# Performance work log

Measured on AMD Instinct MI355X. Metric: run time of the kernel, lower is better.

## Reference

```python
import jax, jax.numpy as jnp
import numpy as np

B, S, D, H = 2, 2048, 1024, 16
DH = D // H
ROPE_BASE = 10000.0


def apply_rope(x):
    # x: [B, H, S, DH]; rotate-half RoPE, base 10000
    half = DH // 2
    inv_freq = 1.0 / (ROPE_BASE ** (jnp.arange(half, dtype=jnp.float32) / half))
    ang = jnp.arange(S, dtype=jnp.float32)[:, None] * inv_freq[None, :]  # [S, half]
    cos = jnp.cos(ang)[None, None]  # [1,1,S,half]
    sin = jnp.sin(ang)[None, None]
    x1, x2 = x[..., :half], x[..., half:]
    return jnp.concatenate([x1 * cos - x2 * sin, x1 * sin + x2 * cos], axis=-1)


def setup_inputs() -> dict:
    key = jax.random.key(0)
    ks = jax.random.split(key, 9)
    w = lambda k: jax.random.normal(k, (D, D), dtype=jnp.float32) * 0.02
    return {
        "x": jax.random.normal(ks[0], (B, S, D), dtype=jnp.float32),
        "Wq": w(ks[1]), "bq": jnp.zeros((D,), jnp.float32),
        "Wk": w(ks[2]), "bk": jnp.zeros((D,), jnp.float32),
        "Wv": w(ks[3]), "bv": jnp.zeros((D,), jnp.float32),
        "Wo": w(ks[4]), "bo": jnp.zeros((D,), jnp.float32),
    }


def reference(x, Wq, bq, Wk, bk, Wv, bv, Wo, bo):
    # projections (W stored as [in, out])
    q = x @ Wq + bq
    k = x @ Wk + bk
    v = x @ Wv + bv
    # [B, S, D] -> [B, H, S, DH]
    to_heads = lambda t: t.reshape(B, S, H, DH).transpose(0, 2, 1, 3)
    q, k, v = to_heads(q), to_heads(k), to_heads(v)
    q = apply_rope(q)
    k = apply_rope(k)
    scores = jnp.einsum("bhqd,bhkd->bhqk", q, k) / jnp.sqrt(jnp.float32(DH))
    causal = jnp.tril(jnp.ones((S, S), dtype=bool))  # [S, S]
    scores = jnp.where(causal[None, None], scores, -jnp.inf)
    probs = jax.nn.softmax(scores, axis=-1)
    ctx = jnp.einsum("bhqk,bhkd->bhqd", probs, v)
    ctx = ctx.transpose(0, 2, 1, 3).reshape(B, S, D)  # concat heads
    return ctx @ Wo + bo
```

## Files before the change

kernel.cpp:

```cpp
#include <hip/hip_runtime.h>
#include <hip/hip_bf16.h>

#define B_  2
#define S_  2048
#define D_  1024
#define H_  16
#define DH_ 64

typedef __attribute__((ext_vector_type(8))) short bf16x8;
typedef __attribute__((ext_vector_type(4))) float f32x4;

__device__ __forceinline__ short f2bf(float f) {
  unsigned int u; __builtin_memcpy(&u, &f, 4);
  u = (u + 0x7FFFu + ((u >> 16) & 1u)) >> 16;
  return (short)u;
}
__device__ __forceinline__ unsigned cvtpk(float a, float b) {
  unsigned r;
  asm("v_cvt_pk_bf16_f32 %0, %1, %2" : "=v"(r) : "v"(a), "v"(b));
  return r;
}

#define GLOAD_LDS16(gp, lp) \
  __builtin_amdgcn_global_load_lds((const __attribute__((address_space(1))) void*)(gp), \
                                   (__attribute__((address_space(3))) void*)(lp), 16, 0, 0)

#define MFMA16(a, b, c) __builtin_amdgcn_mfma_f32_16x16x32_bf16(a, b, c, 0, 0, 0)

union U8 { unsigned u[4]; bf16x8 v; };

__global__ __launch_bounds__(256) void k_cvt(const float* __restrict__ in,
                                             short* __restrict__ out, int n4) {
  int i = blockIdx.x * 256 + threadIdx.x;
  if (i >= n4) return;
  float4 v = ((const float4*)in)[i];
  short4 o; o.x = f2bf(v.x); o.y = f2bf(v.y); o.z = f2bf(v.z); o.w = f2bf(v.w);
  *(short4*)(out + (size_t)i * 4) = o;
}

__global__ __launch_bounds__(256) void k_transpose(const float* __restrict__ W,
                                                   short* __restrict__ Wt) {
  __shared__ float tile[32][33];
  int tx = threadIdx.x, ty = threadIdx.y;
  int bx = blockIdx.x * 32, by = blockIdx.y * 32;
  #pragma unroll
  for (int i = 0; i < 32; i += 8)
    tile[ty + i][tx] = W[(size_t)(by + ty + i) * D_ + bx + tx];
  __syncthreads();
  #pragma unroll
  for (int i = 0; i < 32; i += 8)
    Wt[(size_t)(bx + ty + i) * D_ + by + tx] = f2bf(tile[tx][ty + i]);
}

__global__ __launch_bounds__(256) void k_rope_table(float* __restrict__ cosT,
                                                    float* __restrict__ sinT) {
  int i = blockIdx.x * 256 + threadIdx.x;
  int s = i >> 5, d = i & 31;
  float invf = exp2f(-(float)d * (13.287712379549449f / 32.0f));
  float ang = (float)s * invf;
  cosT[i] = cosf(ang);
  sinT[i] = sinf(ang);
}

__global__ __launch_bounds__(256) void k_gemm_qkv(const short* __restrict__ A,
                                                  const short* __restrict__ Bt,
                                                  const float* __restrict__ bq,
                                                  const float* __restrict__ bk,
                                                  const float* __restrict__ bv,
                                                  const float* __restrict__ cosT,
                                                  const float* __restrict__ sinT,
                                                  short* __restrict__ qb,
                                                  short* __restrict__ kb,
                                                  short* __restrict__ vb) {
  const int K = 1024;
  __shared__ __align__(16) short lA[128 * 32];
  __shared__ __align__(16) short lB[128 * 32];
  const int tid = threadIdx.x;
  const int wid = tid >> 6, lane = tid & 63;
  const int brow = blockIdx.y * 128, bcol = blockIdx.x * 128;
  const int wr = wid >> 1, wc = wid & 1;
  const int g = lane >> 4, c15 = lane & 15;
  const int sr = lane >> 2, scol = (lane & 3) * 8;
  f32x4 acc[4][4] = {};

  for (int kt = 0; kt < K; kt += 32) {
    __syncthreads();
    #pragma unroll
    for (int ch = 0; ch < 2; ++ch) {
      const short* ga = A + (size_t)(brow + ch * 64 + wid * 16 + sr) * K + kt + scol;
      const short* gb = Bt + (size_t)(bcol + ch * 64 + wid * 16 + sr) * K + kt + scol;
      GLOAD_LDS16(ga, &lA[(ch * 64 + wid * 16) * 32]);
      GLOAD_LDS16(gb, &lB[(ch * 64 + wid * 16) * 32]);
    }
    __syncthreads();
    bf16x8 af[4], bfr[4];
    #pragma unroll
    for (int mi = 0; mi < 4; ++mi)
      af[mi] = *(const bf16x8*)&lA[(wr * 64 + mi * 16 + c15) * 32 + g * 8];
    #pragma unroll
    for (int ni = 0; ni < 4; ++ni)
      bfr[ni] = *(const bf16x8*)&lB[(wc * 64 + ni * 16 + c15) * 32 + g * 8];
    #pragma unroll
    for (int mi = 0; mi < 4; ++mi)
      #pragma unroll
      for (int ni = 0; ni < 4; ++ni)
        acc[mi][ni] = MFMA16(af[mi], bfr[ni], acc[mi][ni]);
  }

  const int seg = bcol >> 10;
  const float* bp = (seg == 0) ? bq : (seg == 1) ? bk : bv;
  short* dst = (seg == 0) ? qb : (seg == 1) ? kb : vb;
  const float alpha = (seg == 0) ? 0.18033688f : 1.0f;
  const bool rope = (seg < 2);
  #pragma unroll
  for (int mi = 0; mi < 4; ++mi) {
    #pragma unroll
    for (int ni = 0; ni < 2; ++ni) {
      int col  = bcol + wc * 64 + ni * 16 + c15;
      int lcol = col & 1023;
      int d    = col & 63;
      float b1 = bp[lcol], b2 = bp[lcol + 32];
      #pragma unroll
      for (int r = 0; r < 4; ++r) {
        int row = brow + wr * 64 + mi * 16 + g * 4 + r;
        float x1 = (acc[mi][ni][r]     + b1) * alpha;
        float x2 = (acc[mi][ni + 2][r] + b2) * alpha;
        float o1 = x1, o2 = x2;
        if (rope) {
          int s = row & (S_ - 1);
          float co = cosT[s * 32 + d], si = sinT[s * 32 + d];
          o1 = x1 * co - x2 * si;
          o2 = x1 * si + x2 * co;
        }
        dst[(size_t)row * 1024 + lcol]      = f2bf(o1);
        dst[(size_t)row * 1024 + lcol + 32] = f2bf(o2);
      }
    }
  }
}

__global__ __launch_bounds__(256) void k_gemm(const short* __restrict__ A,
                                              const short* __restrict__ Bt,
                                              const float* __restrict__ bias,
                                              float* __restrict__ out,
                                              int M, int N, int K) {
  __shared__ __align__(16) short lA[128 * 32];
  __shared__ __align__(16) short lB[128 * 32];
  const int tid = threadIdx.x;
  const int wid = tid >> 6, lane = tid & 63;
  const int brow = blockIdx.y * 128, bcol = blockIdx.x * 128;
  const int wr = wid >> 1, wc = wid & 1;
  const int g = lane >> 4, c15 = lane & 15;
  const int sr = lane >> 2, scol = (lane & 3) * 8;
  f32x4 acc[4][4] = {};

  for (int kt = 0; kt < K; kt += 32) {
    __syncthreads();
    #pragma unroll
    for (int ch = 0; ch < 2; ++ch) {
      const short* ga = A + (size_t)(brow + ch * 64 + wid * 16 + sr) * K + kt + scol;
      const short* gb = Bt + (size_t)(bcol + ch * 64 + wid * 16 + sr) * K + kt + scol;
      GLOAD_LDS16(ga, &lA[(ch * 64 + wid * 16) * 32]);
      GLOAD_LDS16(gb, &lB[(ch * 64 + wid * 16) * 32]);
    }
    __syncthreads();
    bf16x8 af[4], bfr[4];
    #pragma unroll
    for (int mi = 0; mi < 4; ++mi)
      af[mi] = *(const bf16x8*)&lA[(wr * 64 + mi * 16 + c15) * 32 + g * 8];
    #pragma unroll
    for (int ni = 0; ni < 4; ++ni)
      bfr[ni] = *(const bf16x8*)&lB[(wc * 64 + ni * 16 + c15) * 32 + g * 8];
    #pragma unroll
    for (int mi = 0; mi < 4; ++mi)
      #pragma unroll
      for (int ni = 0; ni < 4; ++ni)
        acc[mi][ni] = MFMA16(af[mi], bfr[ni], acc[mi][ni]);
  }

  #pragma unroll
  for (int mi = 0; mi < 4; ++mi) {
    #pragma unroll
    for (int ni = 0; ni < 4; ++ni) {
      int col = bcol + wc * 64 + ni * 16 + c15;
      float bv = bias[col];
      #pragma unroll
      for (int r = 0; r < 4; ++r) {
        int row = brow + wr * 64 + mi * 16 + g * 4 + r;
        out[(size_t)row * N + col] = acc[mi][ni][r] + bv;
      }
    }
  }
}

__global__ __launch_bounds__(256) void k_flash(const short* __restrict__ Qb,
                                               const short* __restrict__ Kb,
                                               const short* __restrict__ Vb,
                                               short* __restrict__ Ctx) {
  __shared__ __align__(16) short Vt[2][64][72];
  __shared__ __align__(16) short Kl[2][4096];
  const int bid = blockIdx.x;
  const int qt  = (S_ / 64 - 1) - (bid >> 5);
  const int bh  = bid & 31;
  const int b   = bh >> 4, h = bh & 15;
  const int tid = threadIdx.x, w = tid >> 6, lane = tid & 63;
  const int g   = lane >> 4, c15 = lane & 15;
  const int qg0 = qt * 64 + w * 16;
  const int qabs = qg0 + c15;

  const short* qp = Qb + ((size_t)(b * S_ + qabs)) * D_ + h * DH_ + g * 8;
  bf16x8 qf0 = *(const bf16x8*)qp;
  bf16x8 qf1 = *(const bf16x8*)(qp + 32);

  const int vkv = lane;
  const int vd0 = w * 16;
  const int vcol = vkv ^ (w << 3);
  const short* vrow = Vb + (size_t)b * S_ * D_ + h * DH_ + vd0;

  const short* kbase = Kb + (size_t)b * S_ * D_ + h * DH_;
  const int kidx0 = w * 128 + lane;
  const int kkv0 = kidx0 >> 3, kdb0 = (kidx0 & 7) ^ (kkv0 & 7);
  const int kidx1 = kidx0 + 64;
  const int kkv1 = kidx1 >> 3, kdb1 = (kidx1 & 7) ^ (kkv1 & 7);

  f32x4 o[4] = {};
  float m = -1e30f, l = 0.0f;
  const int nt = qt + 1;

  GLOAD_LDS16(kbase + (size_t)kkv0 * D_ + kdb0 * 8, &Kl[0][(w * 128) * 8]);
  GLOAD_LDS16(kbase + (size_t)kkv1 * D_ + kdb1 * 8, &Kl[0][(w * 128 + 64) * 8]);
  {
    const short* vp = vrow + (size_t)vkv * D_;
    bf16x8 a = *(const bf16x8*)vp;
    bf16x8 c = *(const bf16x8*)(vp + 8);
    #pragma unroll
    for (int j = 0; j < 8; ++j) Vt[0][vd0 + j][vcol] = a[j];
    #pragma unroll
    for (int j = 0; j < 8; ++j) Vt[0][vd0 + 8 + j][vcol] = c[j];
  }
  __syncthreads();

  for (int t = 0; t < nt; ++t) {
    const int kv0 = t * 64;
    bf16x8 nv0, nv1;
    if (t + 1 < nt) {
      const short* kb2 = kbase + (size_t)(kv0 + 64) * D_;
      GLOAD_LDS16(kb2 + (size_t)kkv0 * D_ + kdb0 * 8, &Kl[(t + 1) & 1][(w * 128) * 8]);
      GLOAD_LDS16(kb2 + (size_t)kkv1 * D_ + kdb1 * 8, &Kl[(t + 1) & 1][(w * 128 + 64) * 8]);
      const short* vp = vrow + (size_t)(kv0 + 64 + vkv) * D_;
      nv0 = *(const bf16x8*)vp;
      nv1 = *(const bf16x8*)(vp + 8);
    }
    const short* ks = &Kl[t & 1][0];
    f32x4 s[4] = {};
    __builtin_amdgcn_s_setprio(1);
    #pragma unroll
    for (int n = 0; n < 4; ++n) {
      int krow = (n * 16 + c15) * 64;
      bf16x8 k0 = *(const bf16x8*)&ks[krow + ((g ^ (c15 & 7)) * 8)];
      bf16x8 k1 = *(const bf16x8*)&ks[krow + (((g + 4) ^ (c15 & 7)) * 8)];
      s[n] = MFMA16(k0, qf0, s[n]);
      s[n] = MFMA16(k1, qf1, s[n]);
    }
    __builtin_amdgcn_s_setprio(0);
    if (kv0 + 63 > qg0) {
      #pragma unroll
      for (int n = 0; n < 4; ++n)
        #pragma unroll
        for (int r = 0; r < 4; ++r)
          if (kv0 + n * 16 + g * 4 + r > qabs) s[n][r] = -1e30f;
    }
    float pm = -1e30f;
    #pragma unroll
    for (int n = 0; n < 4; ++n)
      #pragma unroll
      for (int r = 0; r < 4; ++r) pm = fmaxf(pm, s[n][r]);
    pm = fmaxf(pm, __shfl_xor(pm, 16));
    pm = fmaxf(pm, __shfl_xor(pm, 32));
    if (!__all(pm <= m + 8.0f)) {
      float nm = fmaxf(m, pm);
      float corr = exp2f(m - nm);
      m = nm; l *= corr;
      float cf[4];
      #pragma unroll
      for (int r = 0; r < 4; ++r) cf[r] = __shfl(corr, g * 4 + r);
      #pragma unroll
      for (int dblk = 0; dblk < 4; ++dblk)
        #pragma unroll
        for (int r = 0; r < 4; ++r) o[dblk][r] *= cf[r];
    }
    float rs = 0.0f;
    #pragma unroll
    for (int n = 0; n < 4; ++n)
      #pragma unroll
      for (int r = 0; r < 4; ++r) {
        float p = exp2f(s[n][r] - m);
        s[n][r] = p; rs += p;
      }
    rs += __shfl_xor(rs, 16);
    rs += __shfl_xor(rs, 32);
    l += rs;
    unsigned pk[4][2];
    #pragma unroll
    for (int n = 0; n < 4; ++n) {
      pk[n][0] = cvtpk(s[n][0], s[n][1]);
      pk[n][1] = cvtpk(s[n][2], s[n][3]);
    }
    U8 pa[2];
    #pragma unroll
    for (int kh = 0; kh < 2; ++kh) {
      #pragma unroll
      for (int widx = 0; widx < 4; ++widx) {
        int src = (2 * (g & 1) + (widx >> 1)) * 16 + c15;
        unsigned lo = __shfl(pk[2 * kh][widx & 1], src);
        unsigned hi = __shfl(pk[2 * kh + 1][widx & 1], src);
        pa[kh].u[widx] = (g & 2) ? hi : lo;
      }
    }
    __builtin_amdgcn_s_setprio(1);
    #pragma unroll
    for (int kh = 0; kh < 2; ++kh)
      #pragma unroll
      for (int dblk = 0; dblk < 4; ++dblk) {
        bf16x8 vbf = *(const bf16x8*)&Vt[t & 1][dblk * 16 + c15][kh * 32 + ((g ^ dblk) * 8)];
        o[dblk] = MFMA16(pa[kh].v, vbf, o[dblk]);
      }
    __builtin_amdgcn_s_setprio(0);
    if (t + 1 < nt) {
      #pragma unroll
      for (int j = 0; j < 8; ++j) Vt[(t + 1) & 1][vd0 + j][vcol] = nv0[j];
      #pragma unroll
      for (int j = 0; j < 8; ++j) Vt[(t + 1) & 1][vd0 + 8 + j][vcol] = nv1[j];
    }
    __syncthreads();
  }
  float linv = 1.0f / l;
  float lf[4];
  #pragma unroll
  for (int r = 0; r < 4; ++r) lf[r] = __shfl(linv, g * 4 + r);
  #pragma unroll
  for (int dblk = 0; dblk < 4; ++dblk)
    #pragma unroll
    for (int r = 0; r < 4; ++r) {
      int q = qg0 + g * 4 + r;
      Ctx[((size_t)(b * S_ + q)) * D_ + h * DH_ + dblk * 16 + c15] = f2bf(o[dblk][r] * lf[r]);
    }
}

extern "C" void kernel_launch(void* const* d_in, const int* in_sizes, int n_in,
                              void* d_out, int out_size, void* d_ws, size_t ws_size,
                              hipStream_t stream) {
  (void)in_sizes; (void)n_in; (void)out_size; (void)ws_size;
  const float* x  = (const float*)d_in[0];
  const float* Wq = (const float*)d_in[1];
  const float* bq = (const float*)d_in[2];
  const float* Wk = (const float*)d_in[3];
  const float* bk = (const float*)d_in[4];
  const float* Wv = (const float*)d_in[5];
  const float* bv = (const float*)d_in[6];
  const float* Wo = (const float*)d_in[7];
  const float* bo = (const float*)d_in[8];
  float* out = (float*)d_out;
  char* ws = (char*)d_ws;

  const size_t MS = (size_t)B_ * S_;
  short* xb  = (short*)(ws);
  short* wqT = (short*)(ws + (size_t)8 * 1024 * 1024);
  short* wkT = wqT + (size_t)D_ * D_;
  short* wvT = wkT + (size_t)D_ * D_;
  short* woT = wvT + (size_t)D_ * D_;
  short* qb  = (short*)(ws + (size_t)16 * 1024 * 1024);
  short* kb  = qb + MS * D_;
  short* vb  = kb + MS * D_;
  short* ctx = vb + MS * D_;
  float* cosT = (float*)(ws + (size_t)48 * 1024 * 1024);
  float* sinT = cosT + (size_t)S_ * 32;

  k_cvt<<<dim3((unsigned)(MS * D_ / 4 / 256)), 256, 0, stream>>>(x, xb, (int)(MS * D_ / 4));
  dim3 tb(32, 8);
  k_transpose<<<dim3(32, 32), tb, 0, stream>>>(Wq, wqT);
  k_transpose<<<dim3(32, 32), tb, 0, stream>>>(Wk, wkT);
  k_transpose<<<dim3(32, 32), tb, 0, stream>>>(Wv, wvT);
  k_transpose<<<dim3(32, 32), tb, 0, stream>>>(Wo, woT);
  k_rope_table<<<dim3(S_ * 32 / 256), 256, 0, stream>>>(cosT, sinT);
  k_gemm_qkv<<<dim3(24, 32), 256, 0, stream>>>(xb, wqT, bq, bk, bv, cosT, sinT, qb, kb, vb);
  k_flash<<<dim3((S_ / 64) * 32), 256, 0, stream>>>(qb, kb, vb, ctx);
  k_gemm<<<dim3(8, 32), 256, 0, stream>>>(ctx, woT, bo, out, 4096, 1024, 1024);
}
```

Measured before the change: 144.6 us.

## Produce V transposed in a separate GEMM and read it directly in flash attention

V now comes from its own GEMM (Wv^T times x^T), which writes V already transposed ([D, B*S] layout). The flash kernel then loads V fragments straight from global memory instead of staging and transposing them through shared memory. It also skips the whole score/PV path for warps whose rows lie entirely above the causal diagonal. This removes the per-tile LDS transpose writes and the Vt shared buffer, but V fragments now come from global or L2 with less reuse, and the flash kernel is now one launch longer in the chain.

```diff
diff --git a/kernel.cpp b/kernel.cpp
--- a/kernel.cpp
+++ b/kernel.cpp
@@ -66,12 +66,10 @@
                                                   const short* __restrict__ Bt,
                                                   const float* __restrict__ bq,
                                                   const float* __restrict__ bk,
-                                                  const float* __restrict__ bv,
                                                   const float* __restrict__ cosT,
                                                   const float* __restrict__ sinT,
                                                   short* __restrict__ qb,
-                                                  short* __restrict__ kb,
-                                                  short* __restrict__ vb) {
+                                                  short* __restrict__ kb) {
   const int K = 1024;
   __shared__ __align__(16) short lA[128 * 32];
   __shared__ __align__(16) short lB[128 * 32];
@@ -108,10 +106,9 @@
   }
 
   const int seg = bcol >> 10;
-  const float* bp = (seg == 0) ? bq : (seg == 1) ? bk : bv;
-  short* dst = (seg == 0) ? qb : (seg == 1) ? kb : vb;
+  const float* bp = (seg == 0) ? bq : bk;
+  short* dst = (seg == 0) ? qb : kb;
   const float alpha = (seg == 0) ? 0.18033688f : 1.0f;
-  const bool rope = (seg < 2);
   #pragma unroll
   for (int mi = 0; mi < 4; ++mi) {
     #pragma unroll
@@ -125,15 +122,63 @@
         int row = brow + wr * 64 + mi * 16 + g * 4 + r;
         float x1 = (acc[mi][ni][r]     + b1) * alpha;
         float x2 = (acc[mi][ni + 2][r] + b2) * alpha;
-        float o1 = x1, o2 = x2;
-        if (rope) {
-          int s = row & (S_ - 1);
-          float co = cosT[s * 32 + d], si = sinT[s * 32 + d];
-          o1 = x1 * co - x2 * si;
-          o2 = x1 * si + x2 * co;
-        }
-        dst[(size_t)row * 1024 + lcol]      = f2bf(o1);
-        dst[(size_t)row * 1024 + lcol + 32] = f2bf(o2);
+        int s = row & (S_ - 1);
+        float co = cosT[s * 32 + d], si = sinT[s * 32 + d];
+        dst[(size_t)row * 1024 + lcol]      = f2bf(x1 * co - x2 * si);
+        dst[(size_t)row * 1024 + lcol + 32] = f2bf(x1 * si + x2 * co);
+      }
+    }
+  }
+}
+
+__global__ __launch_bounds__(256) void k_gemm_vt(const short* __restrict__ A,
+                                                 const short* __restrict__ Bt,
+                                                 const float* __restrict__ bias,
+                                                 short* __restrict__ out) {
+  const int K = 1024, N = 4096;
+  __shared__ __align__(16) short lA[128 * 32];
+  __shared__ __align__(16) short lB[128 * 32];
+  const int tid = threadIdx.x;
+  const int wid = tid >> 6, lane = tid & 63;
+  const int brow = blockIdx.y * 128, bcol = blockIdx.x * 128;
+  const int wr = wid >> 1, wc = wid & 1;
+  const int g = lane >> 4, c15 = lane & 15;
+  const int sr = lane >> 2, scol = (lane & 3) * 8;
+  f32x4 acc[4][4] = {};
+
+  for (int kt = 0; kt < K; kt += 32) {
+    __syncthreads();
+    #pragma unroll
+    for (int ch = 0; ch < 2; ++ch) {
+      const short* ga = A + (size_t)(brow + ch * 64 + wid * 16 + sr) * K + kt + scol;
+      const short* gb = Bt + (size_t)(bcol + ch * 64 + wid * 16 + sr) * K + kt + scol;
+      GLOAD_LDS16(ga, &lA[(ch * 64 + wid * 16) * 32]);
+      GLOAD_LDS16(gb, &lB[(ch * 64 + wid * 16) * 32]);
+    }
+    __syncthreads();
+    bf16x8 af[4], bfr[4];
+    #pragma unroll
+    for (int mi = 0; mi < 4; ++mi)
+      af[mi] = *(const bf16x8*)&lA[(wr * 64 + mi * 16 + c15) * 32 + g * 8];
+    #pragma unroll
+    for (int ni = 0; ni < 4; ++ni)
+      bfr[ni] = *(const bf16x8*)&lB[(wc * 64 + ni * 16 + c15) * 32 + g * 8];
+    #pragma unroll
+    for (int mi = 0; mi < 4; ++mi)
+      #pragma unroll
+      for (int ni = 0; ni < 4; ++ni)
+        acc[mi][ni] = MFMA16(af[mi], bfr[ni], acc[mi][ni]);
+  }
+
+  #pragma unroll
+  for (int mi = 0; mi < 4; ++mi) {
+    #pragma unroll
+    for (int ni = 0; ni < 4; ++ni) {
+      int col = bcol + wc * 64 + ni * 16 + c15;
+      #pragma unroll
+      for (int r = 0; r < 4; ++r) {
+        int row = brow + wr * 64 + mi * 16 + g * 4 + r;
+        out[(size_t)row * N + col] = f2bf(acc[mi][ni][r] + bias[row]);
       }
     }
   }
@@ -195,9 +240,8 @@
 
 __global__ __launch_bounds__(256) void k_flash(const short* __restrict__ Qb,
                                                const short* __restrict__ Kb,
-                                               const short* __restrict__ Vb,
+                                               const short* __restrict__ Vt,
                                                short* __restrict__ Ctx) {
-  __shared__ __align__(16) short Vt[2][64][72];
   __shared__ __align__(16) short Kl[2][4096];
   const int bid = blockIdx.x;
   const int qt  = (S_ / 64 - 1) - (bid >> 5);
@@ -212,10 +256,7 @@
   bf16x8 qf0 = *(const bf16x8*)qp;
   bf16x8 qf1 = *(const bf16x8*)(qp + 32);
 
-  const int vkv = lane;
-  const int vd0 = w * 16;
-  const int vcol = vkv ^ (w << 3);
-  const short* vrow = Vb + (size_t)b * S_ * D_ + h * DH_ + vd0;
+  const short* vtq = Vt + ((size_t)(h * 64 + c15)) * 4096 + b * 2048 + g * 8;
 
   const short* kbase = Kb + (size_t)b * S_ * D_ + h * DH_;
   const int kidx0 = w * 128 + lane;
@@ -229,108 +270,95 @@
 
   GLOAD_LDS16(kbase + (size_t)kkv0 * D_ + kdb0 * 8, &Kl[0][(w * 128) * 8]);
   GLOAD_LDS16(kbase + (size_t)kkv1 * D_ + kdb1 * 8, &Kl[0][(w * 128 + 64) * 8]);
-  {
-    const short* vp = vrow + (size_t)vkv * D_;
-    bf16x8 a = *(const bf16x8*)vp;
-    bf16x8 c = *(const bf16x8*)(vp + 8);
-    #pragma unroll
-    for (int j = 0; j < 8; ++j) Vt[0][vd0 + j][vcol] = a[j];
-    #pragma unroll
-    for (int j = 0; j < 8; ++j) Vt[0][vd0 + 8 + j][vcol] = c[j];
-  }
   __syncthreads();
 
   for (int t = 0; t < nt; ++t) {
     const int kv0 = t * 64;
-    bf16x8 nv0, nv1;
     if (t + 1 < nt) {
       const short* kb2 = kbase + (size_t)(kv0 + 64) * D_;
       GLOAD_LDS16(kb2 + (size_t)kkv0 * D_ + kdb0 * 8, &Kl[(t + 1) & 1][(w * 128) * 8]);
       GLOAD_LDS16(kb2 + (size_t)kkv1 * D_ + kdb1 * 8, &Kl[(t + 1) & 1][(w * 128 + 64) * 8]);
-      const short* vp = vrow + (size_t)(kv0 + 64 + vkv) * D_;
-      nv0 = *(const bf16x8*)vp;
-      nv1 = *(const bf16x8*)(vp + 8);
-    }
-    const short* ks = &Kl[t & 1][0];
-    f32x4 s[4] = {};
-    __builtin_amdgcn_s_setprio(1);
-    #pragma unroll
-    for (int n = 0; n < 4; ++n) {
-      int krow = (n * 16 + c15) * 64;
-      bf16x8 k0 = *(const bf16x8*)&ks[krow + ((g ^ (c15 & 7)) * 8)];
-      bf16x8 k1 = *(const bf16x8*)&ks[krow + (((g + 4) ^ (c15 & 7)) * 8)];
-      s[n] = MFMA16(k0, qf0, s[n]);
-      s[n] = MFMA16(k1, qf1, s[n]);
-    }
-    __builtin_amdgcn_s_setprio(0);
-    if (kv0 + 63 > qg0) {
+    }
+    if (kv0 <= qg0 + 15) {
+      const short* ks = &Kl[t & 1][0];
+      f32x4 s[4] = {};
+      __builtin_amdgcn_s_setprio(1);
+      #pragma unroll
+      for (int n = 0; n < 4; ++n) {
+        int krow = (n * 16 + c15) * 64;
+        bf16x8 k0 = *(const bf16x8*)&ks[krow + ((g ^ (c15 & 7)) * 8)];
+        bf16x8 k1 = *(const bf16x8*)&ks[krow + (((g + 4) ^ (c15 & 7)) * 8)];
+        s[n] = MFMA16(k0, qf0, s[n]);
+        s[n] = MFMA16(k1, qf1, s[n]);
+      }
+      __builtin_amdgcn_s_setprio(0);
+      bf16x8 vf[2][4];
+      #pragma unroll
+      for (int kh = 0; kh < 2; ++kh)
+        #pragma unroll
+        for (int dblk = 0; dblk < 4; ++dblk)
+          vf[kh][dblk] = *(const bf16x8*)(vtq + (size_t)dblk * 16 * 4096 + kv0 + kh * 32);
+      if (kv0 + 63 > qg0) {
+        #pragma unroll
+        for (int n = 0; n < 4; ++n)
+          #pragma unroll
+          for (int r = 0; r < 4; ++r)
+            if (kv0 + n * 16 + g * 4 + r > qabs) s[n][r] = -1e30f;
+      }
+      float pm = -1e30f;
       #pragma unroll
       for (int n = 0; n < 4; ++n)
         #pragma unroll
-        for (int r = 0; r < 4; ++r)
-          if (kv0 + n * 16 + g * 4 + r > qabs) s[n][r] = -1e30f;
-    }
-    float pm = -1e30f;
-    #pragma unroll
-    for (int n = 0; n < 4; ++n)
-      #pragma unroll
-      for (int r = 0; r < 4; ++r) pm = fmaxf(pm, s[n][r]);
-    pm = fmaxf(pm, __shfl_xor(pm, 16));
-    pm = fmaxf(pm, __shfl_xor(pm, 32));
-    if (!__all(pm <= m + 8.0f)) {
-      float nm = fmaxf(m, pm);
-      float corr = exp2f(m - nm);
-      m = nm; l *= corr;
-      float cf[4];
-      #pragma unroll
-      for (int r = 0; r < 4; ++r) cf[r] = __shfl(corr, g * 4 + r);
-      #pragma unroll
-      for (int dblk = 0; dblk < 4; ++dblk)
-        #pragma unroll
-        for (int r = 0; r < 4; ++r) o[dblk][r] *= cf[r];
-    }
-    float rs = 0.0f;
-    #pragma unroll
-    for (int n = 0; n < 4; ++n)
-      #pragma unroll
-      for (int r = 0; r < 4; ++r) {
-        float p = exp2f(s[n][r] - m);
-        s[n][r] = p; rs += p;
-      }
-    rs += __shfl_xor(rs, 16);
-    rs += __shfl_xor(rs, 32);
-    l += rs;
-    unsigned pk[4][2];
-    #pragma unroll
-    for (int n = 0; n < 4; ++n) {
-      pk[n][0] = cvtpk(s[n][0], s[n][1]);
-      pk[n][1] = cvtpk(s[n][2], s[n][3]);
-    }
-    U8 pa[2];
-    #pragma unroll
-    for (int kh = 0; kh < 2; ++kh) {
-      #pragma unroll
-      for (int widx = 0; widx < 4; ++widx) {
-        int src = (2 * (g & 1) + (widx >> 1)) * 16 + c15;
-        unsigned lo = __shfl(pk[2 * kh][widx & 1], src);
-        unsigned hi = __shfl(pk[2 * kh + 1][widx & 1], src);
-        pa[kh].u[widx] = (g & 2) ? hi : lo;
-      }
-    }
-    __builtin_amdgcn_s_setprio(1);
-    #pragma unroll
-    for (int kh = 0; kh < 2; ++kh)
-      #pragma unroll
-      for (int dblk = 0; dblk < 4; ++dblk) {
-        bf16x8 vbf = *(const bf16x8*)&Vt[t & 1][dblk * 16 + c15][kh * 32 + ((g ^ dblk) * 8)];
-        o[dblk] = MFMA16(pa[kh].v, vbf, o[dblk]);
-      }
-    __builtin_amdgcn_s_setprio(0);
-    if (t + 1 < nt) {
-      #pragma unroll
-      for (int j = 0; j < 8; ++j) Vt[(t + 1) & 1][vd0 + j][vcol] = nv0[j];
-      #pragma unroll
-      for (int j = 0; j < 8; ++j) Vt[(t + 1) & 1][vd0 + 8 + j][vcol] = nv1[j];
+        for (int r = 0; r < 4; ++r) pm = fmaxf(pm, s[n][r]);
+      pm = fmaxf(pm, __shfl_xor(pm, 16));
+      pm = fmaxf(pm, __shfl_xor(pm, 32));
+      if (!__all(pm <= m + 8.0f)) {
+        float nm = fmaxf(m, pm);
+        float corr = exp2f(m - nm);
+        m = nm; l *= corr;
+        float cf[4];
+        #pragma unroll
+        for (int r = 0; r < 4; ++r) cf[r] = __shfl(corr, g * 4 + r);
+        #pragma unroll
+        for (int dblk = 0; dblk < 4; ++dblk)
+          #pragma unroll
+          for (int r = 0; r < 4; ++r) o[dblk][r] *= cf[r];
+      }
+      float rs = 0.0f;
+      #pragma unroll
+      for (int n = 0; n < 4; ++n)
+        #pragma unroll
+        for (int r = 0; r < 4; ++r) {
+          float p = exp2f(s[n][r] - m);
+          s[n][r] = p; rs += p;
+        }
+      rs += __shfl_xor(rs, 16);
+      rs += __shfl_xor(rs, 32);
+      l += rs;
+      unsigned pk[4][2];
+      #pragma unroll
+      for (int n = 0; n < 4; ++n) {
+        pk[n][0] = cvtpk(s[n][0], s[n][1]);
+        pk[n][1] = cvtpk(s[n][2], s[n][3]);
+      }
+      U8 pa[2];
+      #pragma unroll
+      for (int kh = 0; kh < 2; ++kh) {
+        #pragma unroll
+        for (int widx = 0; widx < 4; ++widx) {
+          int src = (2 * (g & 1) + (widx >> 1)) * 16 + c15;
+          unsigned lo = __shfl(pk[2 * kh][widx & 1], src);
+          unsigned hi = __shfl(pk[2 * kh + 1][widx & 1], src);
+          pa[kh].u[widx] = (g & 2) ? hi : lo;
+        }
+      }
+      __builtin_amdgcn_s_setprio(1);
+      #pragma unroll
+      for (int kh = 0; kh < 2; ++kh)
+        #pragma unroll
+        for (int dblk = 0; dblk < 4; ++dblk)
+          o[dblk] = MFMA16(pa[kh].v, vf[kh][dblk], o[dblk]);
+      __builtin_amdgcn_s_setprio(0);
     }
     __syncthreads();
   }
@@ -371,8 +399,8 @@
   short* woT = wvT + (size_t)D_ * D_;
   short* qb  = (short*)(ws + (size_t)16 * 1024 * 1024);
   short* kb  = qb + MS * D_;
-  short* vb  = kb + MS * D_;
-  short* ctx = vb + MS * D_;
+  short* vt  = kb + MS * D_;
+  short* ctx = vt + MS * D_;
   float* cosT = (float*)(ws + (size_t)48 * 1024 * 1024);
   float* sinT = cosT + (size_t)S_ * 32;
 
@@ -383,7 +411,8 @@
   k_transpose<<<dim3(32, 32), tb, 0, stream>>>(Wv, wvT);
   k_transpose<<<dim3(32, 32), tb, 0, stream>>>(Wo, woT);
   k_rope_table<<<dim3(S_ * 32 / 256), 256, 0, stream>>>(cosT, sinT);
-  k_gemm_qkv<<<dim3(24, 32), 256, 0, stream>>>(xb, wqT, bq, bk, bv, cosT, sinT, qb, kb, vb);
-  k_flash<<<dim3((S_ / 64) * 32), 256, 0, stream>>>(qb, kb, vb, ctx);
+  k_gemm_qkv<<<dim3(16, 32), 256, 0, stream>>>(xb, wqT, bq, bk, cosT, sinT, qb, kb);
+  k_gemm_vt<<<dim3(32, 8), 256, 0, stream>>>(wvT, xb, bv, vt);
+  k_flash<<<dim3((S_ / 64) * 32), 256, 0, stream>>>(qb, kb, vt, ctx);
   k_gemm<<<dim3(8, 32), 256, 0, stream>>>(ctx, woT, bo, out, 4096, 1024, 1024);
 }
```

Result: slower. 173.8 us (+20.1%).

## Split long causal query tiles across two flash blocks and merge partials

Applied to the files above, without the earlier changes.

Query tiles 19-31 are now each split into two KV-range halves handled by separate blocks. Each half writes an unnormalized fp32 partial output plus its running max and sum, and a new combine kernel merges the two with log-sum-exp weighting. This evens out the per-block work under the causal mask and adds blocks so the GPU stays busier near the end of the flash kernel, at the cost of an extra launch and fp32 partial traffic. The four weight-transpose launches are also merged into one launch using blockIdx.z.

```diff
diff --git a/kernel.cpp b/kernel.cpp
--- a/kernel.cpp
+++ b/kernel.cpp
@@ -38,9 +38,15 @@
   *(short4*)(out + (size_t)i * 4) = o;
 }
 
-__global__ __launch_bounds__(256) void k_transpose(const float* __restrict__ W,
-                                                   short* __restrict__ Wt) {
+__global__ __launch_bounds__(256) void k_transpose4(const float* __restrict__ W0,
+                                                    const float* __restrict__ W1,
+                                                    const float* __restrict__ W2,
+                                                    const float* __restrict__ W3,
+                                                    short* __restrict__ WtBase) {
   __shared__ float tile[32][33];
+  const float* W = (blockIdx.z == 0) ? W0 : (blockIdx.z == 1) ? W1 :
+                   (blockIdx.z == 2) ? W2 : W3;
+  short* Wt = WtBase + (size_t)blockIdx.z * D_ * D_;
   int tx = threadIdx.x, ty = threadIdx.y;
   int bx = blockIdx.x * 32, by = blockIdx.y * 32;
   #pragma unroll
@@ -196,12 +202,22 @@
 __global__ __launch_bounds__(256) void k_flash(const short* __restrict__ Qb,
                                                const short* __restrict__ Kb,
                                                const short* __restrict__ Vb,
-                                               short* __restrict__ Ctx) {
+                                               short* __restrict__ Ctx,
+                                               float* __restrict__ pO,
+                                               float* __restrict__ pML) {
   __shared__ __align__(16) short Vt[2][64][72];
   __shared__ __align__(16) short Kl[2][4096];
   const int bid = blockIdx.x;
-  const int qt  = (S_ / 64 - 1) - (bid >> 5);
-  const int bh  = bid & 31;
+  const int sched = bid >> 5, bh = bid & 31;
+  int qt, t0, t1, sid = 0; bool split;
+  if (sched < 19) { qt = 18 - sched; t0 = 0; t1 = qt; split = false; }
+  else {
+    int j = sched - 19; qt = 31 - (j >> 1);
+    int h1 = (qt + 2) >> 1;
+    if ((j & 1) == 0) { t0 = h1; t1 = qt; }
+    else              { t0 = 0;  t1 = h1 - 1; }
+    split = true; sid = bh * 26 + j;
+  }
   const int b   = bh >> 4, h = bh & 15;
   const int tid = threadIdx.x, w = tid >> 6, lane = tid & 63;
   const int g   = lane >> 4, c15 = lane & 15;
@@ -225,25 +241,25 @@
 
   f32x4 o[4] = {};
   float m = -1e30f, l = 0.0f;
-  const int nt = qt + 1;
-
-  GLOAD_LDS16(kbase + (size_t)kkv0 * D_ + kdb0 * 8, &Kl[0][(w * 128) * 8]);
-  GLOAD_LDS16(kbase + (size_t)kkv1 * D_ + kdb1 * 8, &Kl[0][(w * 128 + 64) * 8]);
+
   {
-    const short* vp = vrow + (size_t)vkv * D_;
+    const short* kb0 = kbase + (size_t)(t0 * 64) * D_;
+    GLOAD_LDS16(kb0 + (size_t)kkv0 * D_ + kdb0 * 8, &Kl[t0 & 1][(w * 128) * 8]);
+    GLOAD_LDS16(kb0 + (size_t)kkv1 * D_ + kdb1 * 8, &Kl[t0 & 1][(w * 128 + 64) * 8]);
+    const short* vp = vrow + (size_t)(t0 * 64 + vkv) * D_;
     bf16x8 a = *(const bf16x8*)vp;
     bf16x8 c = *(const bf16x8*)(vp + 8);
     #pragma unroll
-    for (int j = 0; j < 8; ++j) Vt[0][vd0 + j][vcol] = a[j];
-    #pragma unroll
-    for (int j = 0; j < 8; ++j) Vt[0][vd0 + 8 + j][vcol] = c[j];
+    for (int j = 0; j < 8; ++j) Vt[t0 & 1][vd0 + j][vcol] = a[j];
+    #pragma unroll
+    for (int j = 0; j < 8; ++j) Vt[t0 & 1][vd0 + 8 + j][vcol] = c[j];
   }
   __syncthreads();
 
-  for (int t = 0; t < nt; ++t) {
+  for (int t = t0; t <= t1; ++t) {
     const int kv0 = t * 64;
     bf16x8 nv0, nv1;
-    if (t + 1 < nt) {
+    if (t + 1 <= t1) {
       const short* kb2 = kbase + (size_t)(kv0 + 64) * D_;
       GLOAD_LDS16(kb2 + (size_t)kkv0 * D_ + kdb0 * 8, &Kl[(t + 1) & 1][(w * 128) * 8]);
       GLOAD_LDS16(kb2 + (size_t)kkv1 * D_ + kdb1 * 8, &Kl[(t + 1) & 1][(w * 128 + 64) * 8]);
@@ -326,7 +342,7 @@
         o[dblk] = MFMA16(pa[kh].v, vbf, o[dblk]);
       }
     __builtin_amdgcn_s_setprio(0);
-    if (t + 1 < nt) {
+    if (t + 1 <= t1) {
       #pragma unroll
       for (int j = 0; j < 8; ++j) Vt[(t + 1) & 1][vd0 + j][vcol] = nv0[j];
       #pragma unroll
@@ -334,17 +350,61 @@
     }
     __syncthreads();
   }
-  float linv = 1.0f / l;
-  float lf[4];
+
+  if (!split) {
+    float linv = 1.0f / l;
+    float lf[4];
+    #pragma unroll
+    for (int r = 0; r < 4; ++r) lf[r] = __shfl(linv, g * 4 + r);
+    #pragma unroll
+    for (int dblk = 0; dblk < 4; ++dblk)
+      #pragma unroll
+      for (int r = 0; r < 4; ++r) {
+        int q = qg0 + g * 4 + r;
+        Ctx[((size_t)(b * S_ + q)) * D_ + h * DH_ + dblk * 16 + c15] = f2bf(o[dblk][r] * lf[r]);
+      }
+  } else {
+    float* po = pO + ((size_t)sid * 64 + w * 16) * 64;
+    #pragma unroll
+    for (int dblk = 0; dblk < 4; ++dblk)
+      #pragma unroll
+      for (int r = 0; r < 4; ++r)
+        po[(g * 4 + r) * 64 + dblk * 16 + c15] = o[dblk][r];
+    if (lane < 16) {
+      pML[(size_t)sid * 128 + w * 16 + lane]      = m;
+      pML[(size_t)sid * 128 + 64 + w * 16 + lane] = l;
+    }
+  }
+}
+
+__global__ __launch_bounds__(256) void k_combine(const float* __restrict__ pO,
+                                                 const float* __restrict__ pML,
+                                                 short* __restrict__ Ctx) {
+  const int p = blockIdx.x;
+  const int qt = 19 + (p >> 5), bh = p & 31;
+  const int b = bh >> 4, h = bh & 15;
+  const int jb = (31 - qt) * 2;
+  const int sidB = bh * 26 + jb;
+  const int sidA = bh * 26 + jb + 1;
+  const int q = threadIdx.x >> 2;
+  const int d0 = (threadIdx.x & 3) * 16;
+  float mA = pML[(size_t)sidA * 128 + q], lA = pML[(size_t)sidA * 128 + 64 + q];
+  float mB = pML[(size_t)sidB * 128 + q], lB = pML[(size_t)sidB * 128 + 64 + q];
+  float M = fmaxf(mA, mB);
+  float wA = exp2f(mA - M), wB = exp2f(mB - M);
+  float inv = 1.0f / (lA * wA + lB * wB);
+  const float* oA = pO + ((size_t)sidA * 64 + q) * 64 + d0;
+  const float* oB = pO + ((size_t)sidB * 64 + q) * 64 + d0;
+  short* cp = Ctx + ((size_t)(b * S_ + qt * 64 + q)) * D_ + h * DH_ + d0;
   #pragma unroll
-  for (int r = 0; r < 4; ++r) lf[r] = __shfl(linv, g * 4 + r);
-  #pragma unroll
-  for (int dblk = 0; dblk < 4; ++dblk)
-    #pragma unroll
-    for (int r = 0; r < 4; ++r) {
-      int q = qg0 + g * 4 + r;
-      Ctx[((size_t)(b * S_ + q)) * D_ + h * DH_ + dblk * 16 + c15] = f2bf(o[dblk][r] * lf[r]);
-    }
+  for (int i = 0; i < 16; i += 4) {
+    float4 a = *(const float4*)(oA + i);
+    float4 c = *(const float4*)(oB + i);
+    cp[i + 0] = f2bf((a.x * wA + c.x * wB) * inv);
+    cp[i + 1] = f2bf((a.y * wA + c.y * wB) * inv);
+    cp[i + 2] = f2bf((a.z * wA + c.z * wB) * inv);
+    cp[i + 3] = f2bf((a.w * wA + c.w * wB) * inv);
+  }
 }
 
 extern "C" void kernel_launch(void* const* d_in, const int* in_sizes, int n_in,
@@ -375,15 +435,14 @@
   short* ctx = vb + MS * D_;
   float* cosT = (float*)(ws + (size_t)48 * 1024 * 1024);
   float* sinT = cosT + (size_t)S_ * 32;
+  float* pO  = (float*)(ws);
+  float* pML = (float*)(ws + (size_t)48 * 1024 * 1024 + 512 * 1024);
 
   k_cvt<<<dim3((unsigned)(MS * D_ / 4 / 256)), 256, 0, stream>>>(x, xb, (int)(MS * D_ / 4));
-  dim3 tb(32, 8);
-  k_transpose<<<dim3(32, 32), tb, 0, stream>>>(Wq, wqT);
-  k_transpose<<<dim3(32, 32), tb, 0, stream>>>(Wk, wkT);
-  k_transpose<<<dim3(32, 32), tb, 0, stream>>>(Wv, wvT);
-  k_transpose<<<dim3(32, 32), tb, 0, stream>>>(Wo, woT);
+  k_transpose4<<<dim3(32, 32, 4), dim3(32, 8), 0, stream>>>(Wq, Wk, Wv, Wo, wqT);
   k_rope_table<<<dim3(S_ * 32 / 256), 256, 0, stream>>>(cosT, sinT);
   k_gemm_qkv<<<dim3(24, 32), 256, 0, stream>>>(xb, wqT, bq, bk, bv, cosT, sinT, qb, kb, vb);
-  k_flash<<<dim3((S_ / 64) * 32), 256, 0, stream>>>(qb, kb, vb, ctx);
+  k_flash<<<dim3(45 * 32), 256, 0, stream>>>(qb, kb, vb, ctx, pO, pML);
+  k_combine<<<dim3(13 * 32), 256, 0, stream>>>(pO, pML, ctx);
   k_gemm<<<dim3(8, 32), 256, 0, stream>>>(ctx, woT, bo, out, 4096, 1024, 1024);
 }
```

Result: faster. 138.5 us (-4.3%).
